# Kernel optimization log

Measured on AMD Instinct MI355X. Metric: run time of the kernel, lower is better.

The kernel has to match this reference:

```python
import jax, jax.numpy as jnp
import numpy as np

NUM_HEADS = 16


def setup_inputs() -> dict:
    key = jax.random.key(0)
    k1, k2, k3 = jax.random.split(key, 3)
    B, S, E = 2, 2048, 1024
    hidden_states = jax.random.normal(k1, (B, S, E), dtype=jnp.float32)
    c_attn_w = jax.random.normal(k2, (E, 3 * E), dtype=jnp.float32) * 0.02
    c_attn_b = jnp.zeros((3 * E,), dtype=jnp.float32)
    c_proj_w = jax.random.normal(k3, (E, E), dtype=jnp.float32) * 0.02
    c_proj_b = jnp.zeros((E,), dtype=jnp.float32)
    return {
        "hidden_states": hidden_states,
        "c_attn_w": c_attn_w,
        "c_attn_b": c_attn_b,
        "c_proj_w": c_proj_w,
        "c_proj_b": c_proj_b,
    }


def reference(hidden_states, c_attn_w, c_attn_b, c_proj_w, c_proj_b):
    B, S, E = hidden_states.shape
    H = NUM_HEADS
    D = E // H
    # Conv1D: qkv projection -> [B, S, 3E]
    qkv = jnp.einsum("bse,ef->bsf", hidden_states, c_attn_w) + c_attn_b
    q, k, v = jnp.split(qkv, 3, axis=-1)
    # split heads -> [B, H, S, D]
    def heads(x):
        return x.reshape(B, S, H, D).transpose(0, 2, 1, 3)
    q, k, v = heads(q), heads(k), heads(v)
    # scaled QK^T -> [B, H, S, S]
    scale = jnp.asarray(D, dtype=q.dtype) ** 0.5
    attn_weights = jnp.einsum("bhqd,bhkd->bhqk", q, k) / scale
    # causal mask (bias buffer): True on/below diagonal
    causal = jnp.tril(jnp.ones((S, S), dtype=bool))
    mask_value = jnp.finfo(attn_weights.dtype).min
    attn_weights = jnp.where(causal[None, None, :, :], attn_weights, mask_value)
    attn_weights = jax.nn.softmax(attn_weights, axis=-1)
    # attn @ V -> merge heads -> [B, S, E]
    attn_out = jnp.einsum("bhqk,bhkd->bhqd", attn_weights, v)
    attn_out = attn_out.transpose(0, 2, 1, 3).reshape(B, S, E)
    # output projection (Conv1D)
    out = jnp.einsum("bse,ef->bsf", attn_out, c_proj_w) + c_proj_b
    return out
```

## Files before the change

kernel.cpp:

```cpp
#include <hip/hip_runtime.h>
#include <stdint.h>

typedef __attribute__((ext_vector_type(8))) __bf16 bf16x8;
typedef __attribute__((ext_vector_type(4))) __bf16 bf16x4;
typedef __attribute__((ext_vector_type(4))) float f32x4;

#define MFMA16(a, b, c) __builtin_amdgcn_mfma_f32_16x16x32_bf16(a, b, c, 0, 0, 0)

__device__ __forceinline__ void async_ld16(const __bf16* g, __bf16* lds_base) {
    __builtin_amdgcn_global_load_lds(
        (const __attribute__((address_space(1))) void*)g,
        (__attribute__((address_space(3))) void*)lds_base, 16, 0, 0);
}

__global__ __launch_bounds__(256) void k_prep(
    const float* __restrict__ hs, const float* __restrict__ w1,
    const float* __restrict__ w2, __bf16* __restrict__ hsb,
    __bf16* __restrict__ w1t, __bf16* __restrict__ w2t) {
    __shared__ __bf16 tile[32][33];
    int bid = blockIdx.x, tid = threadIdx.x;
    if (bid < 4096) {
        int i = (bid * 256 + tid) * 4;
        float4 v = *(const float4*)(hs + i);
        bf16x4 o;
        o.x = (__bf16)v.x; o.y = (__bf16)v.y; o.z = (__bf16)v.z; o.w = (__bf16)v.w;
        *(bf16x4*)(hsb + i) = o;
        return;
    }
    const float* in; __bf16* out; int C, tb;
    if (bid < 7168) { in = w1; out = w1t; C = 3072; tb = bid - 4096; }
    else            { in = w2; out = w2t; C = 1024; tb = bid - 7168; }
    const int R = 1024;
    int ntc = C >> 5;
    int c0 = (tb % ntc) * 32, r0 = (tb / ntc) * 32;
    int tx = tid & 31, ty = tid >> 5;
#pragma unroll
    for (int i = 0; i < 4; i++)
        tile[ty + i * 8][tx] = (__bf16)in[(size_t)(r0 + ty + i * 8) * C + c0 + tx];
    __syncthreads();
#pragma unroll
    for (int i = 0; i < 4; i++)
        out[(size_t)(c0 + ty + i * 8) * R + r0 + tx] = tile[tx][ty + i * 8];
}

__global__ __launch_bounds__(256, 2) void k_gemm_qkv(
    const __bf16* __restrict__ A, const __bf16* __restrict__ Bt,
    const float* __restrict__ bias,
    __bf16* __restrict__ Qo, __bf16* __restrict__ Ko, __bf16* __restrict__ Vo) {
    __shared__ __bf16 As[128 * 32];
    __shared__ __bf16 Bs[128 * 32];
    const int Kd = 1024;
    int n0 = blockIdx.x * 128, m0 = blockIdx.y * 128;
    int tid = threadIdx.x;
    int wv = tid >> 6, lane = tid & 63;
    int wm = (wv >> 1) * 64, wn = (wv & 1) * 64;
    int quad = lane >> 4, l16 = lane & 15;
    int lrow = lane >> 2, lcol = (lane & 3) * 8;
    f32x4 acc[4][4] = {};
    for (int k0 = 0; k0 < Kd; k0 += 32) {
        __syncthreads();
#pragma unroll
        for (int r = 0; r < 2; r++) {
            int row = r * 64 + wv * 16;
            async_ld16(&A[(size_t)(m0 + row + lrow) * Kd + k0 + lcol], &As[row * 32]);
            async_ld16(&Bt[(size_t)(n0 + row + lrow) * Kd + k0 + lcol], &Bs[row * 32]);
        }
        __syncthreads();
        bf16x8 af[4], bfr[4];
#pragma unroll
        for (int i = 0; i < 4; i++)
            af[i] = *(const bf16x8*)(&As[(wm + i * 16 + l16) * 32 + quad * 8]);
#pragma unroll
        for (int j = 0; j < 4; j++)
            bfr[j] = *(const bf16x8*)(&Bs[(wn + j * 16 + l16) * 32 + quad * 8]);
#pragma unroll
        for (int i = 0; i < 4; i++)
#pragma unroll
            for (int j = 0; j < 4; j++)
                acc[i][j] = MFMA16(af[i], bfr[j], acc[i][j]);
    }
#pragma unroll
    for (int i = 0; i < 4; i++) {
#pragma unroll
        for (int j = 0; j < 4; j++) {
            int n = n0 + wn + j * 16 + l16;
            float bv = bias[n];
            int sec = n >> 10, nl = n & 1023;
            int h = nl >> 6, d = nl & 63;
            int mbase = m0 + wm + i * 16 + quad * 4;
            int bb = mbase >> 11, s = mbase & 2047;
            if (sec == 2) {
                bf16x4 v4;
#pragma unroll
                for (int r = 0; r < 4; r++) v4[r] = (__bf16)(acc[i][j][r] + bv);
                *(bf16x4*)(&Vo[((size_t)(bb * 16 + h) * 64 + d) * 2048 + s]) = v4;
            } else {
                __bf16* dst = sec == 0 ? Qo : Ko;
                float scl = (sec == 0) ? 0.1803368801f : 1.0f;
#pragma unroll
                for (int r = 0; r < 4; r++)
                    dst[((size_t)(bb * 16 + h) * 2048 + (s + r)) * 64 + d] =
                        (__bf16)((acc[i][j][r] + bv) * scl);
            }
        }
    }
}

__global__ __launch_bounds__(256, 2) void k_gemm_proj(
    const __bf16* __restrict__ A, const __bf16* __restrict__ Bt,
    const float* __restrict__ bias, float* __restrict__ out) {
    __shared__ __bf16 As[64 * 32];
    __shared__ __bf16 Bs[128 * 32];
    const int Kd = 1024;
    int n0 = blockIdx.x * 128, m0 = blockIdx.y * 64;
    int tid = threadIdx.x;
    int wv = tid >> 6, lane = tid & 63;
    int wm = (wv >> 1) * 32, wn = (wv & 1) * 64;
    int quad = lane >> 4, l16 = lane & 15;
    int lrow = lane >> 2, lcol = (lane & 3) * 8;
    f32x4 acc[2][4] = {};
    for (int k0 = 0; k0 < Kd; k0 += 32) {
        __syncthreads();
        async_ld16(&A[(size_t)(m0 + wv * 16 + lrow) * Kd + k0 + lcol], &As[(wv * 16) * 32]);
#pragma unroll
        for (int r = 0; r < 2; r++) {
            int row = r * 64 + wv * 16;
            async_ld16(&Bt[(size_t)(n0 + row + lrow) * Kd + k0 + lcol], &Bs[row * 32]);
        }
        __syncthreads();
        bf16x8 af[2], bfr[4];
#pragma unroll
        for (int i = 0; i < 2; i++)
            af[i] = *(const bf16x8*)(&As[(wm + i * 16 + l16) * 32 + quad * 8]);
#pragma unroll
        for (int j = 0; j < 4; j++)
            bfr[j] = *(const bf16x8*)(&Bs[(wn + j * 16 + l16) * 32 + quad * 8]);
#pragma unroll
        for (int i = 0; i < 2; i++)
#pragma unroll
            for (int j = 0; j < 4; j++)
                acc[i][j] = MFMA16(af[i], bfr[j], acc[i][j]);
    }
#pragma unroll
    for (int i = 0; i < 2; i++) {
#pragma unroll
        for (int j = 0; j < 4; j++) {
            int n = n0 + wn + j * 16 + l16;
            float bv = bias[n];
#pragma unroll
            for (int r = 0; r < 4; r++) {
                int m = m0 + wm + i * 16 + quad * 4 + r;
                out[(size_t)m * 1024 + n] = acc[i][j][r] + bv;
            }
        }
    }
}

__device__ const int ATT_ORDER[24] = {7, 8, 10, 12, 14, 16, 18, 20, 22, 23, 6, 21,
                                      5, 19, 4, 17, 3, 15, 2, 13, 1, 11, 0, 9};

__global__ __launch_bounds__(256, 3) void k_attn(
    const __bf16* __restrict__ Qg, const __bf16* __restrict__ Kg,
    const __bf16* __restrict__ Vtg, __bf16* __restrict__ Op, float* __restrict__ Lp) {
    __shared__ __bf16 Ksb[2][64 * 64];
    __shared__ __bf16 Vtb[2][64 * 64];
    __shared__ __bf16 Ps[128 * 72];
    int bh = blockIdx.x & 31;
    int slot = ATT_ORDER[blockIdx.x >> 5];
    int t, k0, k1;
    if (slot < 8) { t = slot; k0 = 0; k1 = 2 * t + 2; }
    else { int i2 = slot - 8; t = 8 + (i2 >> 1); k0 = (i2 & 1) * 16; k1 = min(k0 + 16, 2 * t + 2); }
    const __bf16* Qp = Qg + (size_t)bh * 2048 * 64;
    const __bf16* Kp = Kg + (size_t)bh * 2048 * 64;
    const __bf16* Vp = Vtg + (size_t)bh * 64 * 2048;
    int tid = threadIdx.x, wv = tid >> 6, lane = tid & 63;
    int quad = lane >> 4, l16 = lane & 15;
    int rl = lane >> 3, sj = lane & 7;
    int sgo = (sj ^ rl) << 3;
    int swl = l16 & 7;

    bf16x8 qf[2][2];
#pragma unroll
    for (int qn = 0; qn < 2; qn++)
#pragma unroll
        for (int ks = 0; ks < 2; ks++)
            qf[qn][ks] = *(const bf16x8*)(
                &Qp[(size_t)(t * 128 + wv * 32 + qn * 16 + l16) * 64 + ks * 32 + quad * 8]);
    float l_th[2] = {0.f, 0.f};
    f32x4 acc_o[2][4] = {};

    auto stage = [&](int buf, int kt) {
#pragma unroll
        for (int half = 0; half < 2; half++) {
            int r0 = wv * 16 + half * 8;
            async_ld16(&Kp[(size_t)(kt * 64 + r0 + rl) * 64 + sgo], &Ksb[buf][r0 * 64]);
            async_ld16(&Vp[(size_t)(r0 + rl) * 2048 + kt * 64 + sgo], &Vtb[buf][r0 * 64]);
        }
    };

    stage(0, k0);
    __syncthreads();

    for (int kt = k0; kt < k1; kt++) {
        int cur = (kt - k0) & 1;
        if (kt + 1 < k1) stage(cur ^ 1, kt + 1);
        const __bf16* Kc = Ksb[cur];
        const __bf16* Vc = Vtb[cur];
        f32x4 s[2][4] = {};
#pragma unroll
        for (int ks = 0; ks < 2; ks++) {
            bf16x8 kf[4];
#pragma unroll
            for (int i = 0; i < 4; i++)
                kf[i] = *(const bf16x8*)(
                    &Kc[(i * 16 + l16) * 64 + (((ks * 4 + quad) ^ swl) << 3)]);
#pragma unroll
            for (int i = 0; i < 4; i++)
#pragma unroll
                for (int qn = 0; qn < 2; qn++)
                    s[qn][i] = MFMA16(kf[i], qf[qn][ks], s[qn][i]);
        }
#pragma unroll
        for (int qn = 0; qn < 2; qn++) {
            int qmin = t * 128 + wv * 32 + qn * 16;
            if (kt * 64 + 63 > qmin) {
#pragma unroll
                for (int i = 0; i < 4; i++)
#pragma unroll
                    for (int r = 0; r < 4; r++)
                        if (kt * 64 + i * 16 + quad * 4 + r > qmin + l16) s[qn][i][r] = -1e30f;
            }
        }
#pragma unroll
        for (int qn = 0; qn < 2; qn++)
#pragma unroll
            for (int i = 0; i < 4; i++) {
                bf16x4 pk;
#pragma unroll
                for (int r = 0; r < 4; r++) {
                    float p = exp2f(s[qn][i][r]);
                    l_th[qn] += p;
                    pk[r] = (__bf16)p;
                }
                *(bf16x4*)(&Ps[(wv * 32 + qn * 16 + l16) * 72 + i * 16 + quad * 4]) = pk;
            }
#pragma unroll
        for (int ks = 0; ks < 2; ks++) {
            bf16x8 pf[2];
#pragma unroll
            for (int qn = 0; qn < 2; qn++)
                pf[qn] = *(const bf16x8*)(
                    &Ps[(wv * 32 + qn * 16 + l16) * 72 + ks * 32 + quad * 8]);
            bf16x8 vf[4];
#pragma unroll
            for (int i = 0; i < 4; i++)
                vf[i] = *(const bf16x8*)(
                    &Vc[(i * 16 + l16) * 64 + (((ks * 4 + quad) ^ swl) << 3)]);
#pragma unroll
            for (int i = 0; i < 4; i++)
#pragma unroll
                for (int qn = 0; qn < 2; qn++)
                    acc_o[qn][i] = MFMA16(vf[i], pf[qn], acc_o[qn][i]);
        }
        __syncthreads();
    }
    size_t pbase = (size_t)slot * 32 + bh;
#pragma unroll
    for (int qn = 0; qn < 2; qn++) {
        float ls = l_th[qn];
        ls += __shfl_xor(ls, 16);
        ls += __shfl_xor(ls, 32);
        int ql = wv * 32 + qn * 16 + l16;
        if (quad == 0) Lp[pbase * 128 + ql] = ls;
#pragma unroll
        for (int i = 0; i < 4; i++) {
            bf16x4 o4;
#pragma unroll
            for (int r = 0; r < 4; r++) o4[r] = (__bf16)acc_o[qn][i][r];
            *(bf16x4*)(&Op[(pbase * 128 + ql) * 64 + i * 16 + quad * 4]) = o4;
        }
    }
}

__global__ __launch_bounds__(256) void k_attn_combine(
    const __bf16* __restrict__ Op, const float* __restrict__ Lp,
    __bf16* __restrict__ AOb) {
    int gid = blockIdx.x * 256 + threadIdx.x;
    int d4 = gid & 15;
    int q = (gid >> 4) & 2047;
    int bh = gid >> 15;
    int t = q >> 7, ql = q & 127;
    int n = (t <= 7) ? 1 : 2;
    int base = (t <= 7) ? t : 8 + 2 * (t - 8);
    float L = 0.f, o[4] = {};
    for (int c = 0; c < n; c++) {
        size_t idx = (size_t)(base + c) * 32 + bh;
        L += Lp[idx * 128 + ql];
        bf16x4 p4 = *(const bf16x4*)(&Op[(idx * 128 + ql) * 64 + d4 * 4]);
#pragma unroll
        for (int r = 0; r < 4; r++) o[r] += (float)p4[r];
    }
    float inv = 1.f / L;
    int b = bh >> 4, h = bh & 15;
    bf16x4 o4;
#pragma unroll
    for (int r = 0; r < 4; r++) o4[r] = (__bf16)(o[r] * inv);
    *(bf16x4*)(&AOb[((size_t)b * 2048 + q) * 1024 + h * 64 + d4 * 4]) = o4;
}

extern "C" void kernel_launch(void* const* d_in, const int* in_sizes, int n_in,
                              void* d_out, int out_size, void* d_ws, size_t ws_size,
                              hipStream_t stream) {
    const float* hs = (const float*)d_in[0];
    const float* w1 = (const float*)d_in[1];
    const float* b1 = (const float*)d_in[2];
    const float* w2 = (const float*)d_in[3];
    const float* b2 = (const float*)d_in[4];
    float* out = (float*)d_out;

    char* ws = (char*)d_ws;
    __bf16* hsb = (__bf16*)(ws);
    __bf16* w1t = (__bf16*)(ws + (size_t)8 * 1024 * 1024);
    __bf16* w2t = (__bf16*)(ws + (size_t)14 * 1024 * 1024);
    __bf16* Qb  = (__bf16*)(ws + (size_t)16 * 1024 * 1024);
    __bf16* Kb  = (__bf16*)(ws + (size_t)24 * 1024 * 1024);
    __bf16* Vb  = (__bf16*)(ws + (size_t)32 * 1024 * 1024);
    __bf16* AOb = (__bf16*)(ws + (size_t)40 * 1024 * 1024);
    __bf16* Opart = (__bf16*)(ws);
    float*  Lpart = (float*)(ws + (size_t)13 * 1024 * 1024);

    k_prep<<<8192, 256, 0, stream>>>(hs, w1, w2, hsb, w1t, w2t);
    k_gemm_qkv<<<dim3(24, 32), 256, 0, stream>>>(hsb, w1t, b1, Qb, Kb, Vb);
    k_attn<<<768, 256, 0, stream>>>(Qb, Kb, Vb, Opart, Lpart);
    k_attn_combine<<<4096, 256, 0, stream>>>(Opart, Lpart, AOb);
    k_gemm_proj<<<dim3(8, 64), 256, 0, stream>>>(AOb, w2t, b2, out);
}
```

Measured before the change: 181.5 us.

## Remap GEMM blocks per XCD, raise occupancy, and tune attention MFMA priority

The QKV and projection GEMMs now use a 1D grid with block IDs remapped so that each XCD works on a contiguous group of M/N tiles, to improve L2 reuse of A and B. Their launch bounds go from 2 to 3 waves per SIMD. In the attention kernel, the first QK MFMA now takes a zero accumulator instead of needing zero-initialised scores, the row sum is kept as a vector, and s_setprio brackets the MFMA blocks. Tighter register limits at the higher occupancy could cause spills.

```diff
diff --git a/kernel.cpp b/kernel.cpp
--- a/kernel.cpp
+++ b/kernel.cpp
@@ -43,14 +43,18 @@
         out[(size_t)(c0 + ty + i * 8) * R + r0 + tx] = tile[tx][ty + i * 8];
 }
 
-__global__ __launch_bounds__(256, 2) void k_gemm_qkv(
+__global__ __launch_bounds__(256, 3) void k_gemm_qkv(
     const __bf16* __restrict__ A, const __bf16* __restrict__ Bt,
     const float* __restrict__ bias,
     __bf16* __restrict__ Qo, __bf16* __restrict__ Ko, __bf16* __restrict__ Vo) {
     __shared__ __bf16 As[128 * 32];
     __shared__ __bf16 Bs[128 * 32];
     const int Kd = 1024;
-    int n0 = blockIdx.x * 128, m0 = blockIdx.y * 128;
+    int lid = blockIdx.x;
+    int xcd = lid & 7, c = lid >> 3;
+    int mi = (xcd >> 1) * 8 + c / 12;
+    int ni = (xcd & 1) * 12 + c % 12;
+    int n0 = ni * 128, m0 = mi * 128;
     int tid = threadIdx.x;
     int wv = tid >> 6, lane = tid & 63;
     int wm = (wv >> 1) * 64, wn = (wv & 1) * 64;
@@ -106,13 +110,17 @@
     }
 }
 
-__global__ __launch_bounds__(256, 2) void k_gemm_proj(
+__global__ __launch_bounds__(256, 3) void k_gemm_proj(
     const __bf16* __restrict__ A, const __bf16* __restrict__ Bt,
     const float* __restrict__ bias, float* __restrict__ out) {
     __shared__ __bf16 As[64 * 32];
     __shared__ __bf16 Bs[128 * 32];
     const int Kd = 1024;
-    int n0 = blockIdx.x * 128, m0 = blockIdx.y * 64;
+    int lid = blockIdx.x;
+    int xcd = lid & 7, c = lid >> 3;
+    int mi = xcd * 8 + (c >> 3);
+    int ni = c & 7;
+    int n0 = ni * 128, m0 = mi * 64;
     int tid = threadIdx.x;
     int wv = tid >> 6, lane = tid & 63;
     int wm = (wv >> 1) * 32, wn = (wv & 1) * 64;
@@ -186,7 +194,8 @@
         for (int ks = 0; ks < 2; ks++)
             qf[qn][ks] = *(const bf16x8*)(
                 &Qp[(size_t)(t * 128 + wv * 32 + qn * 16 + l16) * 64 + ks * 32 + quad * 8]);
-    float l_th[2] = {0.f, 0.f};
+    const f32x4 zf = {0.f, 0.f, 0.f, 0.f};
+    f32x4 lacc[2] = {zf, zf};
     f32x4 acc_o[2][4] = {};
 
     auto stage = [&](int buf, int kt) {
@@ -206,7 +215,7 @@
         if (kt + 1 < k1) stage(cur ^ 1, kt + 1);
         const __bf16* Kc = Ksb[cur];
         const __bf16* Vc = Vtb[cur];
-        f32x4 s[2][4] = {};
+        f32x4 s[2][4];
 #pragma unroll
         for (int ks = 0; ks < 2; ks++) {
             bf16x8 kf[4];
@@ -214,11 +223,13 @@
             for (int i = 0; i < 4; i++)
                 kf[i] = *(const bf16x8*)(
                     &Kc[(i * 16 + l16) * 64 + (((ks * 4 + quad) ^ swl) << 3)]);
+            __builtin_amdgcn_s_setprio(1);
 #pragma unroll
             for (int i = 0; i < 4; i++)
 #pragma unroll
                 for (int qn = 0; qn < 2; qn++)
-                    s[qn][i] = MFMA16(kf[i], qf[qn][ks], s[qn][i]);
+                    s[qn][i] = MFMA16(kf[i], qf[qn][ks], ks == 0 ? zf : s[qn][i]);
+            __builtin_amdgcn_s_setprio(0);
         }
 #pragma unroll
         for (int qn = 0; qn < 2; qn++) {
@@ -235,13 +246,13 @@
         for (int qn = 0; qn < 2; qn++)
 #pragma unroll
             for (int i = 0; i < 4; i++) {
+                f32x4 pe;
+#pragma unroll
+                for (int r = 0; r < 4; r++) pe[r] = exp2f(s[qn][i][r]);
+                lacc[qn] += pe;
                 bf16x4 pk;
 #pragma unroll
-                for (int r = 0; r < 4; r++) {
-                    float p = exp2f(s[qn][i][r]);
-                    l_th[qn] += p;
-                    pk[r] = (__bf16)p;
-                }
+                for (int r = 0; r < 4; r++) pk[r] = (__bf16)pe[r];
                 *(bf16x4*)(&Ps[(wv * 32 + qn * 16 + l16) * 72 + i * 16 + quad * 4]) = pk;
             }
 #pragma unroll
@@ -256,18 +267,20 @@
             for (int i = 0; i < 4; i++)
                 vf[i] = *(const bf16x8*)(
                     &Vc[(i * 16 + l16) * 64 + (((ks * 4 + quad) ^ swl) << 3)]);
+            __builtin_amdgcn_s_setprio(1);
 #pragma unroll
             for (int i = 0; i < 4; i++)
 #pragma unroll
                 for (int qn = 0; qn < 2; qn++)
                     acc_o[qn][i] = MFMA16(vf[i], pf[qn], acc_o[qn][i]);
+            __builtin_amdgcn_s_setprio(0);
         }
         __syncthreads();
     }
     size_t pbase = (size_t)slot * 32 + bh;
 #pragma unroll
     for (int qn = 0; qn < 2; qn++) {
-        float ls = l_th[qn];
+        float ls = lacc[qn][0] + lacc[qn][1] + lacc[qn][2] + lacc[qn][3];
         ls += __shfl_xor(ls, 16);
         ls += __shfl_xor(ls, 32);
         int ql = wv * 32 + qn * 16 + l16;
@@ -330,8 +343,8 @@
     float*  Lpart = (float*)(ws + (size_t)13 * 1024 * 1024);
 
     k_prep<<<8192, 256, 0, stream>>>(hs, w1, w2, hsb, w1t, w2t);
-    k_gemm_qkv<<<dim3(24, 32), 256, 0, stream>>>(hsb, w1t, b1, Qb, Kb, Vb);
+    k_gemm_qkv<<<768, 256, 0, stream>>>(hsb, w1t, b1, Qb, Kb, Vb);
     k_attn<<<768, 256, 0, stream>>>(Qb, Kb, Vb, Opart, Lpart);
     k_attn_combine<<<4096, 256, 0, stream>>>(Opart, Lpart, AOb);
-    k_gemm_proj<<<dim3(8, 64), 256, 0, stream>>>(AOb, w2t, b2, out);
-}
+    k_gemm_proj<<<512, 256, 0, stream>>>(AOb, w2t, b2, out);
+}
```

Result: no change. 181.7 us (+0.1%).
